# Optimization experiments

Hardware: AMD Instinct MI355X
Metric: run time of the kernel (lower is better)

## Reference

```python
import jax, jax.numpy as jnp
import numpy as np

EMBED_DIM = 1024
NUM_HEADS = 16
HEAD_DIM = EMBED_DIM // NUM_HEADS
TGT_LEN = 1024
SRC_LEN = 1024
BSZ = 4


def setup_inputs() -> dict:
    key = jax.random.key(0)
    ks = jax.random.split(key, 7)
    query = jax.random.normal(ks[0], (TGT_LEN, BSZ, EMBED_DIM), dtype=jnp.float32)
    key_t = jax.random.normal(ks[1], (SRC_LEN, BSZ, EMBED_DIM), dtype=jnp.float32)
    # hard 0/1 multiplicative mask applied post-softmax
    hard_attention = jax.random.randint(ks[2], (BSZ, TGT_LEN, SRC_LEN), 0, 2).astype(jnp.float32)
    # xavier_uniform_ on [3E, E]
    limit = float(np.sqrt(6.0 / (3 * EMBED_DIM + EMBED_DIM)))
    in_proj_weight = jax.random.uniform(ks[3], (3 * EMBED_DIM, EMBED_DIM), dtype=jnp.float32,
                                        minval=-limit, maxval=limit)
    in_proj_bias = jnp.zeros((3 * EMBED_DIM,), dtype=jnp.float32)
    limit_o = float(np.sqrt(1.0 / EMBED_DIM))
    out_proj_weight = jax.random.uniform(ks[4], (EMBED_DIM, EMBED_DIM), dtype=jnp.float32,
                                         minval=-limit_o, maxval=limit_o)
    out_proj_bias = jnp.zeros((EMBED_DIM,), dtype=jnp.float32)
    return {
        "query": query,
        "key": key_t,
        "hard_attention": hard_attention,
        "in_proj_weight": in_proj_weight,
        "in_proj_bias": in_proj_bias,
        "out_proj_weight": out_proj_weight,
        "out_proj_bias": out_proj_bias,
    }


def reference(query, key, hard_attention, in_proj_weight, in_proj_bias,
              out_proj_weight, out_proj_bias):
    tgt_len, bsz, embed_dim = query.shape
    src_len = key.shape[0]
    h, hd = NUM_HEADS, embed_dim // NUM_HEADS
    scaling = float(hd) ** -0.5

    # QKV projections (F.linear uses y = x @ W.T + b)
    wq = in_proj_weight[:embed_dim]
    wkv = in_proj_weight[embed_dim:]
    bq = in_proj_bias[:embed_dim]
    bkv = in_proj_bias[embed_dim:]
    q = jnp.einsum('tbe,fe->tbf', query, wq) + bq          # [T,B,E]
    kv = jnp.einsum('sbe,fe->sbf', key, wkv) + bkv          # [S,B,2E]
    k, v = jnp.split(kv, 2, axis=-1)

    q = (q * scaling).reshape(tgt_len, bsz, h, hd).transpose(1, 2, 0, 3)  # [B,H,T,D]
    k = k.reshape(src_len, bsz, h, hd).transpose(1, 2, 0, 3)              # [B,H,S,D]
    v = v.reshape(src_len, bsz, h, hd).transpose(1, 2, 0, 3)              # [B,H,S,D]

    scores = jnp.einsum('bhtd,bhsd->bhts', q, k)            # [B,H,T,S]
    attn = jax.nn.softmax(scores, axis=-1)
    # dropout_p = 0.0 -> identity
    attn = attn * hard_attention[:, None, :, :]             # post-softmax hard mask

    out = jnp.einsum('bhts,bhsd->bhtd', attn, v)            # [B,H,T,D]
    out = out.transpose(2, 0, 1, 3).reshape(tgt_len, bsz, embed_dim)
    out = jnp.einsum('tbe,fe->tbf', out, out_proj_weight) + out_proj_bias

    avg_weights = attn.sum(axis=1) / h                      # [B,T,S]
    return (out, avg_weights)
```

## Files before the change

### kernel.cpp

```cpp
#include <hip/hip_runtime.h>
#include <cstdint>
#include <cstddef>

typedef __bf16 bf16x8 __attribute__((ext_vector_type(8)));
typedef float  f32x4  __attribute__((ext_vector_type(4)));
typedef unsigned short u16x8 __attribute__((ext_vector_type(8)));

__device__ __forceinline__ uint16_t f2bf(float f) {
  uint32_t u = __float_as_uint(f);
  u += 0x7fffu + ((u >> 16) & 1u);
  return (uint16_t)(u >> 16);
}
__device__ __forceinline__ float bf2f(uint16_t u) {
  return __uint_as_float((uint32_t)u << 16);
}

__device__ __forceinline__ f32x4 mfma16(bf16x8 a, bf16x8 b, f32x4 c) {
  return __builtin_amdgcn_mfma_f32_16x16x32_bf16(a, b, c, 0, 0, 0);
}

#define GLD_TO_LDS16(gptr, lptr)                                                   \
  __builtin_amdgcn_global_load_lds(                                                \
      (const __attribute__((address_space(1))) void*)(gptr),                       \
      (__attribute__((address_space(3))) void*)(lptr), 16, 0, 0)

__global__ void cvt_all(const float* __restrict__ q, const float* __restrict__ k,
                        const float* __restrict__ w, const float* __restrict__ wo,
                        uint16_t* __restrict__ Xq, uint16_t* __restrict__ Xk,
                        uint16_t* __restrict__ Wb, uint16_t* __restrict__ Wob) {
  int i = blockIdx.x * blockDim.x + threadIdx.x;
  const float* src;
  uint16_t* dst;
  int off;
  if (i < 1048576)      { src = q;  dst = Xq;  off = i; }
  else if (i < 2097152) { src = k;  dst = Xk;  off = i - 1048576; }
  else if (i < 2883584) { src = w;  dst = Wb;  off = i - 2097152; }
  else                  { src = wo; dst = Wob; off = i - 2883584; }
  float4 v = ((const float4*)src)[off];
  ushort4 o;
  o.x = f2bf(v.x); o.y = f2bf(v.y); o.z = f2bf(v.z); o.w = f2bf(v.w);
  ((ushort4*)dst)[off] = o;
}

__global__ void bitpack(const float* __restrict__ hard, uint32_t* __restrict__ bits) {
  int i = blockIdx.x * 256 + threadIdx.x;
  unsigned long long m = __ballot(hard[i] != 0.0f);
  if ((threadIdx.x & 63) == 0) {
    int w = i >> 5;
    bits[w]     = (uint32_t)m;
    bits[w + 1] = (uint32_t)(m >> 32);
  }
}

__global__ __launch_bounds__(256)
void gemm_qkv(const uint16_t* __restrict__ Xq, const uint16_t* __restrict__ Xk,
              const uint16_t* __restrict__ Wb, const float* __restrict__ ipb,
              uint16_t* __restrict__ Qb, uint16_t* __restrict__ Kb,
              uint16_t* __restrict__ Vt) {
  __shared__ __align__(16) uint16_t As[128 * 32];
  __shared__ __align__(16) uint16_t Bs[128 * 32];
  const int tid  = threadIdx.x;
  const int wave = tid >> 6, lane = tid & 63;
  const int quad = lane >> 4, l16 = lane & 15;

  const int bid = blockIdx.x;
  const uint16_t *A, *B;
  const float* bias;
  int bm, bn, mode;
  if (bid < 256) {
    mode = 0; A = Xq; B = Wb; bias = ipb;
    bm = bid >> 3; bn = bid & 7;
  } else {
    mode = 1; A = Xk; B = Wb + (1 << 20); bias = ipb + 1024;
    int t = bid - 256; bm = t >> 4; bn = t & 15;
  }
  const int wm = (wave >> 1) << 6, wn = (wave & 1) << 6;
  const int K = 1024;

  f32x4 acc[4][4] = {};

  for (int k0 = 0; k0 < K; k0 += 32) {
    __syncthreads();
#pragma unroll
    for (int j = 0; j < 2; j++) {
      int c   = wave * 128 + j * 64 + lane;
      int row = c >> 2, kc = c & 3;
      const uint16_t* ga = A + (size_t)(bm * 128 + row) * K + k0 + kc * 8;
      GLD_TO_LDS16(ga, As + (size_t)(wave * 128 + j * 64) * 8);
      const uint16_t* gb = B + (size_t)(bn * 128 + row) * K + k0 + kc * 8;
      GLD_TO_LDS16(gb, Bs + (size_t)(wave * 128 + j * 64) * 8);
    }
    __syncthreads();

    bf16x8 af[4], bfr[4];
#pragma unroll
    for (int i = 0; i < 4; i++) {
      af[i]  = *(const bf16x8*)(As + (wm + i * 16 + l16) * 32 + quad * 8);
      bfr[i] = *(const bf16x8*)(Bs + (wn + i * 16 + l16) * 32 + quad * 8);
    }
#pragma unroll
    for (int mi = 0; mi < 4; mi++)
#pragma unroll
      for (int ni = 0; ni < 4; ni++)
        acc[mi][ni] = mfma16(af[mi], bfr[ni], acc[mi][ni]);
  }

#pragma unroll
  for (int mi = 0; mi < 4; mi++)
#pragma unroll
    for (int ni = 0; ni < 4; ni++)
#pragma unroll
      for (int r = 0; r < 4; r++) {
        int gi = bm * 128 + wm + mi * 16 + quad * 4 + r;
        int gf = bn * 128 + wn + ni * 16 + l16;
        float c = acc[mi][ni][r] + bias[gf];
        if (mode == 0) {
          c *= 0.125f;
          int t = gi >> 2, b = gi & 3, h = gf >> 6, d = gf & 63;
          Qb[((((size_t)b * 16 + h) * 1024 + t) << 6) + d] = f2bf(c);
        } else {
          int s = gi >> 2, b = gi & 3;
          if (gf < 1024) {
            int h = gf >> 6, d = gf & 63;
            Kb[((((size_t)b * 16 + h) * 1024 + s) << 6) + d] = f2bf(c);
          } else {
            int fv = gf - 1024, h = fv >> 6, d = fv & 63;
            Vt[((((size_t)b * 16 + h) * 64 + d) << 10) + s] = f2bf(c);
          }
        }
      }
}

__global__ __launch_bounds__(256)
void gemm_out(const uint16_t* __restrict__ A, const uint16_t* __restrict__ B,
              const float* __restrict__ bias, float* __restrict__ o32) {
  __shared__ __align__(16) uint16_t As[64 * 32];
  __shared__ __align__(16) uint16_t Bs[128 * 32];
  const int tid  = threadIdx.x;
  const int wave = tid >> 6, lane = tid & 63;
  const int quad = lane >> 4, l16 = lane & 15;
  const int bm = blockIdx.x >> 3, bn = blockIdx.x & 7;
  const int wm = (wave >> 1) << 5, wn = (wave & 1) << 6;
  const int K = 1024;

  f32x4 acc[2][4] = {};

  for (int k0 = 0; k0 < K; k0 += 32) {
    __syncthreads();
    {
      int c   = wave * 64 + lane;
      int row = c >> 2, kc = c & 3;
      const uint16_t* ga = A + (size_t)(bm * 64 + row) * K + k0 + kc * 8;
      GLD_TO_LDS16(ga, As + (size_t)(wave * 64) * 8);
    }
#pragma unroll
    for (int j = 0; j < 2; j++) {
      int c   = wave * 128 + j * 64 + lane;
      int row = c >> 2, kc = c & 3;
      const uint16_t* gb = B + (size_t)(bn * 128 + row) * K + k0 + kc * 8;
      GLD_TO_LDS16(gb, Bs + (size_t)(wave * 128 + j * 64) * 8);
    }
    __syncthreads();

    bf16x8 af[2], bfr[4];
#pragma unroll
    for (int i = 0; i < 2; i++)
      af[i] = *(const bf16x8*)(As + (wm + i * 16 + l16) * 32 + quad * 8);
#pragma unroll
    for (int i = 0; i < 4; i++)
      bfr[i] = *(const bf16x8*)(Bs + (wn + i * 16 + l16) * 32 + quad * 8);
#pragma unroll
    for (int mi = 0; mi < 2; mi++)
#pragma unroll
      for (int ni = 0; ni < 4; ni++)
        acc[mi][ni] = mfma16(af[mi], bfr[ni], acc[mi][ni]);
  }

#pragma unroll
  for (int mi = 0; mi < 2; mi++)
#pragma unroll
    for (int ni = 0; ni < 4; ni++)
#pragma unroll
      for (int r = 0; r < 4; r++) {
        int gi = bm * 64 + wm + mi * 16 + quad * 4 + r;
        int gf = bn * 128 + wn + ni * 16 + l16;
        o32[(size_t)gi * 1024 + gf] = acc[mi][ni][r] + bias[gf];
      }
}

__global__ __launch_bounds__(256, 2)
void attn_kernel(const uint16_t* __restrict__ qb, const uint16_t* __restrict__ kb,
                 const uint16_t* __restrict__ vtb, const uint32_t* __restrict__ bits,
                 uint16_t* __restrict__ attn_out, float* __restrict__ rlout) {
  __shared__ __align__(16) uint16_t Ks[128 * 72];
  __shared__ __align__(16) uint16_t Vs[64 * 136];
  __shared__ __align__(16) uint16_t P[4][16 * 140];
  const int PS = 140;

  const int bid = blockIdx.x;
  const int xcd = bid & 7, j = bid >> 3;
  const int slab = xcd * 8 + (j >> 4);
  const int b = slab >> 4, h = slab & 15;
  const int t0 = (j & 15) << 6;
  const int tid = threadIdx.x, wave = tid >> 6, lane = tid & 63;
  const int quad = lane >> 4, l16 = lane & 15;
  const int tw = t0 + wave * 16;
  const size_t bh = (size_t)b * 16 + h;
  uint16_t* Pw = P[wave];

  const uint16_t* qrow = qb + ((bh << 10) + tw + l16) * 64;
  bf16x8 aq0 = *(const bf16x8*)(qrow + quad * 8);
  bf16x8 aq1 = *(const bf16x8*)(qrow + 32 + quad * 8);

  f32x4 acc[4] = {};
  float sm[4] = {0.f, 0.f, 0.f, 0.f};

  const int kRow = tid >> 3, kCol = (tid & 7) * 8;
  const int vRow = tid >> 4, vCol = (tid & 15) * 8;

  for (int sc = 0; sc < 8; sc++) {
    u16x8 kreg[4], vreg[4];
    const uint16_t* kbase = kb + (((bh << 10) + sc * 128) << 6);
#pragma unroll
    for (int r = 0; r < 4; r++)
      kreg[r] = *(const u16x8*)(kbase + (r * 256 + tid) * 8);
#pragma unroll
    for (int r = 0; r < 4; r++)
      vreg[r] = *(const u16x8*)(vtb + (((bh << 6) + r * 16 + vRow) << 10) +
                                sc * 128 + vCol);

    __syncthreads();
#pragma unroll
    for (int r = 0; r < 4; r++)
      *(u16x8*)(Ks + (r * 32 + kRow) * 72 + kCol) = kreg[r];
#pragma unroll
    for (int r = 0; r < 4; r++)
      *(u16x8*)(Vs + (r * 16 + vRow) * 136 + vCol) = vreg[r];
    __syncthreads();

    uint32_t wsh[4][4];
#pragma unroll
    for (int r = 0; r < 4; r++) {
      uint4 u = *(const uint4*)(bits +
                 (((size_t)(b << 10) + tw + quad * 4 + r) << 5) + sc * 4);
      wsh[r][0] = u.x >> l16; wsh[r][1] = u.y >> l16;
      wsh[r][2] = u.z >> l16; wsh[r][3] = u.w >> l16;
    }

#pragma unroll
    for (int n = 0; n < 8; n++) {
      const uint16_t* krow = Ks + (n * 16 + l16) * 72;
      bf16x8 bk0 = *(const bf16x8*)(krow + quad * 8);
      bf16x8 bk1 = *(const bf16x8*)(krow + 32 + quad * 8);
      f32x4 c = {};
      c = mfma16(aq0, bk0, c);
      c = mfma16(aq1, bk1, c);
#pragma unroll
      for (int r = 0; r < 4; r++) {
        float e = __expf(c[r]);
        sm[r] += e;
        float em = ((wsh[r][n >> 1] >> ((n & 1) * 16)) & 1u) ? e : 0.f;
        Pw[(quad * 4 + r) * PS + n * 16 + l16] = f2bf(em);
      }
    }

#pragma unroll
    for (int kc = 0; kc < 4; kc++) {
      bf16x8 ap = *(const bf16x8*)(Pw + l16 * PS + kc * 32 + quad * 8);
#pragma unroll
      for (int dt = 0; dt < 4; dt++) {
        bf16x8 bv = *(const bf16x8*)(Vs + (dt * 16 + l16) * 136 +
                                     kc * 32 + quad * 8);
        acc[dt] = mfma16(ap, bv, acc[dt]);
      }
    }
  }

  float rl[4];
#pragma unroll
  for (int r = 0; r < 4; r++) {
    float s = sm[r];
#pragma unroll
    for (int off = 1; off < 16; off <<= 1) s += __shfl_xor(s, off);
    rl[r] = 1.0f / s;
  }
  if (l16 == 0) {
#pragma unroll
    for (int r = 0; r < 4; r++)
      rlout[(bh << 10) + tw + quad * 4 + r] = rl[r];
  }

#pragma unroll
  for (int dt = 0; dt < 4; dt++)
#pragma unroll
    for (int r = 0; r < 4; r++) {
      float o = acc[dt][r] * rl[r];
      attn_out[((size_t)(tw + quad * 4 + r) * 4 + b) * 1024 +
               h * 64 + dt * 16 + l16] = f2bf(o);
    }
}

__global__ __launch_bounds__(256, 2)
void avg_kernel(const uint16_t* __restrict__ qb, const uint16_t* __restrict__ kb,
                const float* __restrict__ rlin, const uint32_t* __restrict__ bits,
                float* __restrict__ avgout) {
  __shared__ __align__(16) uint16_t Ks[128 * 72];

  const int bid = blockIdx.x;
  const int xcd = bid & 7, j = bid >> 3;
  const int b  = xcd >> 1;
  const int t0 = ((xcd & 1) * 8 + (j >> 3)) << 6;
  const int s0 = (j & 7) << 7;
  const int tid = threadIdx.x, wave = tid >> 6, lane = tid & 63;
  const int quad = lane >> 4, l16 = lane & 15;
  const int tw = t0 + wave * 16;
  const int kRow = tid >> 3, kCol = (tid & 7) * 8;

  uint32_t wsh[4][4];
#pragma unroll
  for (int r = 0; r < 4; r++) {
    uint4 u = *(const uint4*)(bits +
               (((size_t)(b << 10) + tw + quad * 4 + r) << 5) + (s0 >> 5));
    wsh[r][0] = u.x >> l16; wsh[r][1] = u.y >> l16;
    wsh[r][2] = u.z >> l16; wsh[r][3] = u.w >> l16;
  }

  float av[8][4] = {};

  for (int hh = 0; hh < 16; hh++) {
    const size_t bh = (size_t)b * 16 + hh;

    u16x8 kreg[4];
    const uint16_t* kbase = kb + (((bh << 10) + s0) << 6);
#pragma unroll
    for (int r = 0; r < 4; r++)
      kreg[r] = *(const u16x8*)(kbase + (r * 256 + tid) * 8);
    __syncthreads();
#pragma unroll
    for (int r = 0; r < 4; r++)
      *(u16x8*)(Ks + (r * 32 + kRow) * 72 + kCol) = kreg[r];
    __syncthreads();

    const uint16_t* qrow = qb + ((bh << 10) + tw + l16) * 64;
    bf16x8 aq0 = *(const bf16x8*)(qrow + quad * 8);
    bf16x8 aq1 = *(const bf16x8*)(qrow + 32 + quad * 8);
    float rl[4];
#pragma unroll
    for (int r = 0; r < 4; r++)
      rl[r] = rlin[(bh << 10) + tw + quad * 4 + r];

#pragma unroll
    for (int n = 0; n < 8; n++) {
      const uint16_t* krow = Ks + (n * 16 + l16) * 72;
      bf16x8 bk0 = *(const bf16x8*)(krow + quad * 8);
      bf16x8 bk1 = *(const bf16x8*)(krow + 32 + quad * 8);
      f32x4 c = {};
      c = mfma16(aq0, bk0, c);
      c = mfma16(aq1, bk1, c);
#pragma unroll
      for (int r = 0; r < 4; r++)
        av[n][r] += __expf(c[r]) * rl[r];
    }
  }

#pragma unroll
  for (int n = 0; n < 8; n++)
#pragma unroll
    for (int r = 0; r < 4; r++) {
      float m = ((wsh[r][n >> 1] >> ((n & 1) * 16)) & 1u) ? 0.0625f : 0.f;
      avgout[((size_t)(b << 10) + tw + quad * 4 + r) * 1024 +
             s0 + n * 16 + l16] = av[n][r] * m;
    }
}

extern "C" void kernel_launch(void* const* d_in, const int* in_sizes, int n_in,
                              void* d_out, int out_size, void* d_ws, size_t ws_size,
                              hipStream_t stream) {
  const float* query = (const float*)d_in[0];
  const float* key   = (const float*)d_in[1];
  const float* hard  = (const float*)d_in[2];
  const float* ipw   = (const float*)d_in[3];
  const float* ipb   = (const float*)d_in[4];
  const float* opw   = (const float*)d_in[5];
  const float* opb   = (const float*)d_in[6];

  char* ws = (char*)d_ws;
  const size_t MB = 1ull << 20;
  uint16_t* Xq  = (uint16_t*)(ws + 0);
  uint16_t* Xk  = (uint16_t*)(ws + 8 * MB);
  uint16_t* Wb  = (uint16_t*)(ws + 16 * MB);
  uint16_t* Wob = (uint16_t*)(ws + 22 * MB);
  uint16_t* Qb  = (uint16_t*)(ws + 24 * MB);
  uint16_t* Kb  = (uint16_t*)(ws + 32 * MB);
  uint16_t* Vt  = (uint16_t*)(ws + 40 * MB);
  uint16_t* AO  = Xq;

  float* out = (float*)d_out;
  float* avg = out + 4194304;
  uint32_t* bits  = (uint32_t*)out;
  float*    rlbuf = out + 131072;

  cvt_all<<<12288, 256, 0, stream>>>(query, key, ipw, opw, Xq, Xk, Wb, Wob);
  bitpack<<<16384, 256, 0, stream>>>(hard, bits);

  gemm_qkv<<<768, 256, 0, stream>>>(Xq, Xk, Wb, ipb, Qb, Kb, Vt);

  attn_kernel<<<1024, 256, 0, stream>>>(Qb, Kb, Vt, bits, AO, rlbuf);

  avg_kernel<<<512, 256, 0, stream>>>(Qb, Kb, rlbuf, bits, avg);

  gemm_out<<<512, 256, 0, stream>>>(AO, Wob, opb, out);
}
```

Before: 271.5 us.

## Double tile rows per wave, swizzle LDS, prefetch K/V, transpose MFMA outputs

The attention kernel now processes 128 query rows per block (32 per wave, two MFMA row sets), so each K/V tile loaded into LDS is reused twice as much and the grid is halved. Padded LDS layouts are replaced with XOR-swizzled layouts to avoid bank conflicts. The next K/V chunk and mask bits are prefetched into registers while computing. MFMA operands are swapped so each lane holds four consecutive columns, which allows packed bf16 conversion and vectorized stores of P, the output and the averaged weights. The avg kernel gets the same swizzle, prefetch and vectorized float4 output. The cost is higher register pressure, fewer blocks and a more complex index mapping.

```diff
diff --git a/kernel.cpp b/kernel.cpp
--- a/kernel.cpp
+++ b/kernel.cpp
@@ -13,6 +13,11 @@
 }
 __device__ __forceinline__ float bf2f(uint16_t u) {
   return __uint_as_float((uint32_t)u << 16);
+}
+__device__ __forceinline__ uint32_t cvtpk(float lo, float hi) {
+  uint32_t r;
+  asm("v_cvt_pk_bf16_f32 %0, %1, %2" : "=v"(r) : "v"(lo), "v"(hi));
+  return r;
 }
 
 __device__ __forceinline__ f32x4 mfma16(bf16x8 a, bf16x8 b, f32x4 c) {
@@ -192,119 +197,141 @@
 void attn_kernel(const uint16_t* __restrict__ qb, const uint16_t* __restrict__ kb,
                  const uint16_t* __restrict__ vtb, const uint32_t* __restrict__ bits,
                  uint16_t* __restrict__ attn_out, float* __restrict__ rlout) {
-  __shared__ __align__(16) uint16_t Ks[128 * 72];
-  __shared__ __align__(16) uint16_t Vs[64 * 136];
-  __shared__ __align__(16) uint16_t P[4][16 * 140];
-  const int PS = 140;
+  __shared__ __align__(16) uint16_t Ks[128 * 64];
+  __shared__ __align__(16) uint16_t Vs[64 * 128];
+  __shared__ __align__(16) uint16_t Pb[4 * 32 * 128];
 
   const int bid = blockIdx.x;
   const int xcd = bid & 7, j = bid >> 3;
-  const int slab = xcd * 8 + (j >> 4);
+  const int slab = xcd * 8 + (j >> 3);
   const int b = slab >> 4, h = slab & 15;
-  const int t0 = (j & 15) << 6;
+  const int t0 = (j & 7) << 7;
   const int tid = threadIdx.x, wave = tid >> 6, lane = tid & 63;
   const int quad = lane >> 4, l16 = lane & 15;
-  const int tw = t0 + wave * 16;
+  const int sw = (l16 & 7) << 4;
   const size_t bh = (size_t)b * 16 + h;
-  uint16_t* Pw = P[wave];
-
-  const uint16_t* qrow = qb + ((bh << 10) + tw + l16) * 64;
-  bf16x8 aq0 = *(const bf16x8*)(qrow + quad * 8);
-  bf16x8 aq1 = *(const bf16x8*)(qrow + 32 + quad * 8);
-
-  f32x4 acc[4] = {};
-  float sm[4] = {0.f, 0.f, 0.f, 0.f};
-
-  const int kRow = tid >> 3, kCol = (tid & 7) * 8;
-  const int vRow = tid >> 4, vCol = (tid & 15) * 8;
+  const int tw = t0 + wave * 32;
+  const int ta = tw + l16, tb = ta + 16;
+  char* PwA = (char*)(Pb + wave * (32 * 128)) + l16 * 256;
+  char* PwB = PwA + 16 * 256;
+
+  const uint16_t* qA = qb + ((bh << 10) + ta) * 64;
+  bf16x8 aqA0 = *(const bf16x8*)(qA + quad * 8);
+  bf16x8 aqA1 = *(const bf16x8*)(qA + 32 + quad * 8);
+  bf16x8 aqB0 = *(const bf16x8*)(qA + 1024 + quad * 8);
+  bf16x8 aqB1 = *(const bf16x8*)(qA + 1024 + 32 + quad * 8);
+
+  f32x4 accA[4] = {}, accB[4] = {};
+  float smA = 0.f, smB = 0.f;
+
+  const int kr = tid >> 3, kc8 = tid & 7;
+  const int vr = tid >> 4, vc16 = tid & 15;
+
+  const uint32_t* bA = bits + (((size_t)(b << 10) + ta) << 5);
+  const uint32_t* bB = bits + (((size_t)(b << 10) + tb) << 5);
+
+  u16x8 kreg[4], vreg[4];
+#pragma unroll
+  for (int r = 0; r < 4; r++)
+    kreg[r] = *(const u16x8*)(kb + (bh << 16) + (size_t)(r * 256 + tid) * 8);
+#pragma unroll
+  for (int r = 0; r < 4; r++)
+    vreg[r] = *(const u16x8*)(vtb + (((bh << 6) + r * 16 + vr) << 10) + vc16 * 8);
+  uint4 uA = *(const uint4*)bA;
+  uint4 uB = *(const uint4*)bB;
 
   for (int sc = 0; sc < 8; sc++) {
-    u16x8 kreg[4], vreg[4];
-    const uint16_t* kbase = kb + (((bh << 10) + sc * 128) << 6);
-#pragma unroll
-    for (int r = 0; r < 4; r++)
-      kreg[r] = *(const u16x8*)(kbase + (r * 256 + tid) * 8);
-#pragma unroll
-    for (int r = 0; r < 4; r++)
-      vreg[r] = *(const u16x8*)(vtb + (((bh << 6) + r * 16 + vRow) << 10) +
-                                sc * 128 + vCol);
-
-    __syncthreads();
-#pragma unroll
-    for (int r = 0; r < 4; r++)
-      *(u16x8*)(Ks + (r * 32 + kRow) * 72 + kCol) = kreg[r];
-#pragma unroll
-    for (int r = 0; r < 4; r++)
-      *(u16x8*)(Vs + (r * 16 + vRow) * 136 + vCol) = vreg[r];
-    __syncthreads();
-
-    uint32_t wsh[4][4];
+    uint32_t wA[4] = {uA.x >> (quad * 4), uA.y >> (quad * 4),
+                      uA.z >> (quad * 4), uA.w >> (quad * 4)};
+    uint32_t wB[4] = {uB.x >> (quad * 4), uB.y >> (quad * 4),
+                      uB.z >> (quad * 4), uB.w >> (quad * 4)};
+
+    __syncthreads();
 #pragma unroll
     for (int r = 0; r < 4; r++) {
-      uint4 u = *(const uint4*)(bits +
-                 (((size_t)(b << 10) + tw + quad * 4 + r) << 5) + sc * 4);
-      wsh[r][0] = u.x >> l16; wsh[r][1] = u.y >> l16;
-      wsh[r][2] = u.z >> l16; wsh[r][3] = u.w >> l16;
-    }
-
-#pragma unroll
-    for (int n = 0; n < 8; n++) {
-      const uint16_t* krow = Ks + (n * 16 + l16) * 72;
-      bf16x8 bk0 = *(const bf16x8*)(krow + quad * 8);
-      bf16x8 bk1 = *(const bf16x8*)(krow + 32 + quad * 8);
-      f32x4 c = {};
-      c = mfma16(aq0, bk0, c);
-      c = mfma16(aq1, bk1, c);
+      const int row = r * 32 + kr;
+      *(u16x8*)((char*)Ks + row * 128 + ((kc8 * 16) ^ ((row & 7) << 4))) = kreg[r];
+    }
+#pragma unroll
+    for (int r = 0; r < 4; r++) {
+      const int row = r * 16 + vr;
+      *(u16x8*)((char*)Vs + row * 256 + ((vc16 * 16) ^ ((row & 7) << 4))) = vreg[r];
+    }
+    __syncthreads();
+
+    if (sc < 7) {
+      const uint16_t* kbase = kb + (bh << 16) + (size_t)(sc + 1) * 8192;
+#pragma unroll
+      for (int r = 0; r < 4; r++)
+        kreg[r] = *(const u16x8*)(kbase + (size_t)(r * 256 + tid) * 8);
+#pragma unroll
+      for (int r = 0; r < 4; r++)
+        vreg[r] = *(const u16x8*)(vtb + (((bh << 6) + r * 16 + vr) << 10) +
+                                  (sc + 1) * 128 + vc16 * 8);
+      uA = *(const uint4*)(bA + (sc + 1) * 4);
+      uB = *(const uint4*)(bB + (sc + 1) * 4);
+    }
+
+#pragma unroll
+    for (int nn = 0; nn < 8; nn++) {
+      const char* kbp = (const char*)Ks + (nn * 16 + l16) * 128;
+      bf16x8 bk0 = *(const bf16x8*)(kbp + ((quad * 16) ^ sw));
+      bf16x8 bk1 = *(const bf16x8*)(kbp + ((64 + quad * 16) ^ sw));
+      f32x4 cA = {}, cB = {};
+      cA = mfma16(bk0, aqA0, cA); cA = mfma16(bk1, aqA1, cA);
+      cB = mfma16(bk0, aqB0, cB); cB = mfma16(bk1, aqB1, cB);
+      const uint32_t mA = wA[nn >> 1] >> ((nn & 1) * 16);
+      const uint32_t mB = wB[nn >> 1] >> ((nn & 1) * 16);
+      float eA[4], eB[4];
 #pragma unroll
       for (int r = 0; r < 4; r++) {
-        float e = __expf(c[r]);
-        sm[r] += e;
-        float em = ((wsh[r][n >> 1] >> ((n & 1) * 16)) & 1u) ? e : 0.f;
-        Pw[(quad * 4 + r) * PS + n * 16 + l16] = f2bf(em);
+        eA[r] = __expf(cA[r]); smA += eA[r];
+        eB[r] = __expf(cB[r]); smB += eB[r];
+        eA[r] = ((mA >> r) & 1) ? eA[r] : 0.f;
+        eB[r] = ((mB >> r) & 1) ? eB[r] : 0.f;
       }
+      const int pc = (nn * 32 + quad * 8) ^ sw;
+      *(uint2*)(PwA + pc) = make_uint2(cvtpk(eA[0], eA[1]), cvtpk(eA[2], eA[3]));
+      *(uint2*)(PwB + pc) = make_uint2(cvtpk(eB[0], eB[1]), cvtpk(eB[2], eB[3]));
     }
 
 #pragma unroll
     for (int kc = 0; kc < 4; kc++) {
-      bf16x8 ap = *(const bf16x8*)(Pw + l16 * PS + kc * 32 + quad * 8);
+      const int pcb = (kc * 64 + quad * 16) ^ sw;
+      bf16x8 apA = *(const bf16x8*)(PwA + pcb);
+      bf16x8 apB = *(const bf16x8*)(PwB + pcb);
 #pragma unroll
       for (int dt = 0; dt < 4; dt++) {
-        bf16x8 bv = *(const bf16x8*)(Vs + (dt * 16 + l16) * 136 +
-                                     kc * 32 + quad * 8);
-        acc[dt] = mfma16(ap, bv, acc[dt]);
+        bf16x8 bv = *(const bf16x8*)((const char*)Vs + (dt * 16 + l16) * 256 +
+                                     ((kc * 64 + quad * 16) ^ sw));
+        accA[dt] = mfma16(bv, apA, accA[dt]);
+        accB[dt] = mfma16(bv, apB, accB[dt]);
       }
     }
   }
 
-  float rl[4];
-#pragma unroll
-  for (int r = 0; r < 4; r++) {
-    float s = sm[r];
-#pragma unroll
-    for (int off = 1; off < 16; off <<= 1) s += __shfl_xor(s, off);
-    rl[r] = 1.0f / s;
-  }
-  if (l16 == 0) {
-#pragma unroll
-    for (int r = 0; r < 4; r++)
-      rlout[(bh << 10) + tw + quad * 4 + r] = rl[r];
-  }
-
-#pragma unroll
-  for (int dt = 0; dt < 4; dt++)
-#pragma unroll
-    for (int r = 0; r < 4; r++) {
-      float o = acc[dt][r] * rl[r];
-      attn_out[((size_t)(tw + quad * 4 + r) * 4 + b) * 1024 +
-               h * 64 + dt * 16 + l16] = f2bf(o);
-    }
+  smA += __shfl_xor(smA, 16); smA += __shfl_xor(smA, 32);
+  smB += __shfl_xor(smB, 16); smB += __shfl_xor(smB, 32);
+  const float rlA = 1.0f / smA, rlB = 1.0f / smB;
+  if (quad == 0) rlout[(bh << 10) + ta] = rlA;
+  if (quad == 1) rlout[(bh << 10) + tb] = rlB;
+
+#pragma unroll
+  for (int dt = 0; dt < 4; dt++) {
+    uint2 oA = make_uint2(cvtpk(accA[dt][0] * rlA, accA[dt][1] * rlA),
+                          cvtpk(accA[dt][2] * rlA, accA[dt][3] * rlA));
+    *(uint2*)(attn_out + ((size_t)(ta * 4 + b) << 10) + h * 64 + dt * 16 + quad * 4) = oA;
+    uint2 oB = make_uint2(cvtpk(accB[dt][0] * rlB, accB[dt][1] * rlB),
+                          cvtpk(accB[dt][2] * rlB, accB[dt][3] * rlB));
+    *(uint2*)(attn_out + ((size_t)(tb * 4 + b) << 10) + h * 64 + dt * 16 + quad * 4) = oB;
+  }
 }
 
 __global__ __launch_bounds__(256, 2)
 void avg_kernel(const uint16_t* __restrict__ qb, const uint16_t* __restrict__ kb,
                 const float* __restrict__ rlin, const uint32_t* __restrict__ bits,
                 float* __restrict__ avgout) {
-  __shared__ __align__(16) uint16_t Ks[128 * 72];
+  __shared__ __align__(16) uint16_t Ks[128 * 64];
 
   const int bid = blockIdx.x;
   const int xcd = bid & 7, j = bid >> 3;
@@ -313,64 +340,69 @@
   const int s0 = (j & 7) << 7;
   const int tid = threadIdx.x, wave = tid >> 6, lane = tid & 63;
   const int quad = lane >> 4, l16 = lane & 15;
-  const int tw = t0 + wave * 16;
-  const int kRow = tid >> 3, kCol = (tid & 7) * 8;
-
-  uint32_t wsh[4][4];
-#pragma unroll
-  for (int r = 0; r < 4; r++) {
-    uint4 u = *(const uint4*)(bits +
-               (((size_t)(b << 10) + tw + quad * 4 + r) << 5) + (s0 >> 5));
-    wsh[r][0] = u.x >> l16; wsh[r][1] = u.y >> l16;
-    wsh[r][2] = u.z >> l16; wsh[r][3] = u.w >> l16;
-  }
+  const int sw = (l16 & 7) << 4;
+  const int tr = t0 + wave * 16 + l16;
+  const int kr = tid >> 3, kc8 = tid & 7;
+
+  uint4 u = *(const uint4*)(bits + (((size_t)(b << 10) + tr) << 5) + (s0 >> 5));
+  uint32_t w4[4] = {u.x >> (quad * 4), u.y >> (quad * 4),
+                    u.z >> (quad * 4), u.w >> (quad * 4)};
 
   float av[8][4] = {};
 
+  u16x8 kreg[4];
+  {
+    const uint16_t* kb0 = kb + ((((size_t)b * 16) << 10) + s0) * 64;
+#pragma unroll
+    for (int r = 0; r < 4; r++)
+      kreg[r] = *(const u16x8*)(kb0 + (size_t)(r * 256 + tid) * 8);
+  }
+
   for (int hh = 0; hh < 16; hh++) {
+    __syncthreads();
+#pragma unroll
+    for (int r = 0; r < 4; r++) {
+      const int row = r * 32 + kr;
+      *(u16x8*)((char*)Ks + row * 128 + ((kc8 * 16) ^ ((row & 7) << 4))) = kreg[r];
+    }
+    __syncthreads();
+    if (hh < 15) {
+      const uint16_t* kb2 = kb + ((((size_t)b * 16 + hh + 1) << 10) + s0) * 64;
+#pragma unroll
+      for (int r = 0; r < 4; r++)
+        kreg[r] = *(const u16x8*)(kb2 + (size_t)(r * 256 + tid) * 8);
+    }
+
     const size_t bh = (size_t)b * 16 + hh;
-
-    u16x8 kreg[4];
-    const uint16_t* kbase = kb + (((bh << 10) + s0) << 6);
-#pragma unroll
-    for (int r = 0; r < 4; r++)
-      kreg[r] = *(const u16x8*)(kbase + (r * 256 + tid) * 8);
-    __syncthreads();
-#pragma unroll
-    for (int r = 0; r < 4; r++)
-      *(u16x8*)(Ks + (r * 32 + kRow) * 72 + kCol) = kreg[r];
-    __syncthreads();
-
-    const uint16_t* qrow = qb + ((bh << 10) + tw + l16) * 64;
+    const uint16_t* qrow = qb + ((bh << 10) + tr) * 64;
     bf16x8 aq0 = *(const bf16x8*)(qrow + quad * 8);
     bf16x8 aq1 = *(const bf16x8*)(qrow + 32 + quad * 8);
-    float rl[4];
-#pragma unroll
-    for (int r = 0; r < 4; r++)
-      rl[r] = rlin[(bh << 10) + tw + quad * 4 + r];
+    const float rl = rlin[(bh << 10) + tr];
 
 #pragma unroll
     for (int n = 0; n < 8; n++) {
-      const uint16_t* krow = Ks + (n * 16 + l16) * 72;
-      bf16x8 bk0 = *(const bf16x8*)(krow + quad * 8);
-      bf16x8 bk1 = *(const bf16x8*)(krow + 32 + quad * 8);
+      const char* kbp = (const char*)Ks + (n * 16 + l16) * 128;
+      bf16x8 bk0 = *(const bf16x8*)(kbp + ((quad * 16) ^ sw));
+      bf16x8 bk1 = *(const bf16x8*)(kbp + ((64 + quad * 16) ^ sw));
       f32x4 c = {};
-      c = mfma16(aq0, bk0, c);
-      c = mfma16(aq1, bk1, c);
-#pragma unroll
-      for (int r = 0; r < 4; r++)
-        av[n][r] += __expf(c[r]) * rl[r];
-    }
-  }
-
-#pragma unroll
-  for (int n = 0; n < 8; n++)
-#pragma unroll
-    for (int r = 0; r < 4; r++) {
-      float m = ((wsh[r][n >> 1] >> ((n & 1) * 16)) & 1u) ? 0.0625f : 0.f;
-      avgout[((size_t)(b << 10) + tw + quad * 4 + r) * 1024 +
-             s0 + n * 16 + l16] = av[n][r] * m;
-    }
+      c = mfma16(bk0, aq0, c);
+      c = mfma16(bk1, aq1, c);
+#pragma unroll
+      for (int r = 0; r < 4; r++) av[n][r] += __expf(c[r]) * rl;
+    }
+  }
+
+  float* orow = avgout + ((size_t)(b << 10) + tr) * 1024 + s0 + quad * 4;
+#pragma unroll
+  for (int n = 0; n < 8; n++) {
+    const uint32_t m = w4[n >> 1] >> ((n & 1) * 16);
+    float4 f;
+    f.x = av[n][0] * (((m >> 0) & 1) ? 0.0625f : 0.f);
+    f.y = av[n][1] * (((m >> 1) & 1) ? 0.0625f : 0.f);
+    f.z = av[n][2] * (((m >> 2) & 1) ? 0.0625f : 0.f);
+    f.w = av[n][3] * (((m >> 3) & 1) ? 0.0625f : 0.f);
+    *(float4*)(orow + n * 16) = f;
+  }
 }
 
 extern "C" void kernel_launch(void* const* d_in, const int* in_sizes, int n_in,
@@ -405,7 +437,7 @@
 
   gemm_qkv<<<768, 256, 0, stream>>>(Xq, Xk, Wb, ipb, Qb, Kb, Vt);
 
-  attn_kernel<<<1024, 256, 0, stream>>>(Qb, Kb, Vt, bits, AO, rlbuf);
+  attn_kernel<<<512, 256, 0, stream>>>(Qb, Kb, Vt, bits, AO, rlbuf);
 
   avg_kernel<<<512, 256, 0, stream>>>(Qb, Kb, rlbuf, bits, avg);
 
```

Result: faster. 242.0 us (-10.9%).
